# Performance work log

Hardware: AMD Instinct MI355X
Metric: run time of the kernel (lower is better)

Reference implementation:

```python
import jax, jax.numpy as jnp
import numpy as np

B, H, W, C = 32, 64, 64, 256


def setup_inputs() -> dict:
    key = jax.random.key(0)
    kq, kk, kv = jax.random.split(key, 3)
    query = jax.random.normal(kq, (B, H, W, C), dtype=jnp.float32)
    keys = jax.random.normal(kk, (B, H, W, C), dtype=jnp.float32)
    values = jax.random.normal(kv, (B, H, W, C), dtype=jnp.float32)
    return {"query": query, "keys": keys, "values": values}


def reference(query, keys, values):
    # A[b,q,k] = sum_{h,w} query[b,h,w,q] * keys[b,h,w,k]
    scores = jnp.einsum("bhwq,bhwk->bqk", query, keys)
    attn = jax.nn.softmax(scores, axis=-1)  # softmax over keys axis
    # out[b,q,h,w] = sum_k attn[b,q,k] * values[b,h,w,k]
    out = jnp.einsum("bqk,bhwk->bqhw", attn, values)
    return out
```

## Files before the change

kernel.cpp:

```cpp
#include <hip/hip_runtime.h>
#include <hip/hip_bf16.h>

#define B_  32
#define HW_ 4096
#define C_  256
#define S_LDS 40

using bf16x8 = __attribute__((ext_vector_type(8))) short;
using f32x4  = __attribute__((ext_vector_type(4))) float;
using u32x4  = __attribute__((ext_vector_type(4))) uint;

__device__ __forceinline__ ushort f2bf_rn(float x) {
    uint u = __builtin_bit_cast(uint, x);
    u += 0x7FFFu + ((u >> 16) & 1u);
    return (ushort)(u >> 16);
}
__device__ __forceinline__ uint pk_bf2(float a, float b) {
    return ((uint)f2bf_rn(b) << 16) | (uint)f2bf_rn(a);
}
__device__ __forceinline__ uint pk_rtz(float x0, float x1) {
    return __builtin_amdgcn_perm(__builtin_bit_cast(uint, x1),
                                 __builtin_bit_cast(uint, x0), 0x07060302u);
}
__device__ __forceinline__ void split2_rtz(float x0, float x1, uint& hi2, uint& lo2) {
    uint u0 = __builtin_bit_cast(uint, x0), u1 = __builtin_bit_cast(uint, x1);
    hi2 = __builtin_amdgcn_perm(u1, u0, 0x07060302u);
    float h0 = __builtin_bit_cast(float, u0 & 0xFFFF0000u);
    float h1 = __builtin_bit_cast(float, u1 & 0xFFFF0000u);
    lo2 = pk_rtz(x0 - h0, x1 - h1);
}

__global__ __launch_bounds__(256, 4) void scores_kernel(const float* __restrict__ qg,
                                                        const float* __restrict__ kg,
                                                        float* __restrict__ scores) {
    int x  = blockIdx.x;
    int s  = x & 7;
    int tn = (x >> 3) & 3;
    int tm = (x >> 5) & 1;
    int b  = x >> 6;

    __shared__ __align__(16) ushort Qhi[128 * S_LDS], Qlo[128 * S_LDS];
    __shared__ __align__(16) ushort Khi[64 * S_LDS],  Klo[64 * S_LDS];

    int tid = threadIdx.x, lane = tid & 63, w = tid >> 6;
    int m0 = (w >> 1) * 64;
    int n0 = (w & 1) * 32;
    int g = lane >> 4, r16 = lane & 15;

    int cq = tid & 127;
    int hq = (tid >> 7) * 16;
    int ck = tid & 63;
    int hk = (tid >> 6) * 8;

    const float* qcol = qg + (size_t)b * HW_ * C_ + tm * 128 + cq;
    const float* kcol = kg + (size_t)b * HW_ * C_ + tn * 64 + ck;

    f32x4 acc[4][2];
#pragma unroll
    for (int i = 0; i < 4; ++i)
#pragma unroll
        for (int j = 0; j < 2; ++j) acc[i][j] = (f32x4){0.f, 0.f, 0.f, 0.f};

#define LOAD_QK(qr, kr, itv) {                                                 \
        int hw0 = s * 512 + (itv) * 32;                                        \
        const float* qp = qcol + (size_t)(hw0 + hq) * C_;                      \
        _Pragma("unroll")                                                      \
        for (int j = 0; j < 16; ++j) qr[j] = qp[(size_t)j * C_];               \
        const float* kp = kcol + (size_t)(hw0 + hk) * C_;                      \
        _Pragma("unroll")                                                      \
        for (int j = 0; j < 8; ++j) kr[j] = kp[(size_t)j * C_];                \
    }

#define CONVERT_STORE(qr, kr) {                                                \
        uint qh[8], ql[8];                                                     \
        _Pragma("unroll")                                                      \
        for (int p = 0; p < 8; ++p) split2_rtz(qr[2*p], qr[2*p+1], qh[p], ql[p]); \
        int qb_ = cq * S_LDS + hq;                                             \
        *reinterpret_cast<u32x4*>(&Qhi[qb_])     = (u32x4){qh[0], qh[1], qh[2], qh[3]}; \
        *reinterpret_cast<u32x4*>(&Qhi[qb_ + 8]) = (u32x4){qh[4], qh[5], qh[6], qh[7]}; \
        *reinterpret_cast<u32x4*>(&Qlo[qb_])     = (u32x4){ql[0], ql[1], ql[2], ql[3]}; \
        *reinterpret_cast<u32x4*>(&Qlo[qb_ + 8]) = (u32x4){ql[4], ql[5], ql[6], ql[7]}; \
        uint kh[4], kl[4];                                                     \
        _Pragma("unroll")                                                      \
        for (int p = 0; p < 4; ++p) split2_rtz(kr[2*p], kr[2*p+1], kh[p], kl[p]); \
        int kb_ = ck * S_LDS + hk;                                             \
        *reinterpret_cast<u32x4*>(&Khi[kb_]) = (u32x4){kh[0], kh[1], kh[2], kh[3]}; \
        *reinterpret_cast<u32x4*>(&Klo[kb_]) = (u32x4){kl[0], kl[1], kl[2], kl[3]}; \
    }

#define MFMA_PHASE() {                                                         \
        __builtin_amdgcn_s_setprio(1);                                         \
        bf16x8 ahi[4], alo[4];                                                 \
        _Pragma("unroll")                                                      \
        for (int mi = 0; mi < 4; ++mi) {                                       \
            int off = (m0 + mi * 16 + r16) * S_LDS + g * 8;                    \
            ahi[mi] = *reinterpret_cast<const bf16x8*>(&Qhi[off]);             \
            alo[mi] = *reinterpret_cast<const bf16x8*>(&Qlo[off]);             \
        }                                                                      \
        _Pragma("unroll")                                                      \
        for (int ni = 0; ni < 2; ++ni) {                                       \
            int off = (n0 + ni * 16 + r16) * S_LDS + g * 8;                    \
            bf16x8 bhi = *reinterpret_cast<const bf16x8*>(&Khi[off]);          \
            bf16x8 blo = *reinterpret_cast<const bf16x8*>(&Klo[off]);          \
            _Pragma("unroll")                                                  \
            for (int mi = 0; mi < 4; ++mi) {                                   \
                acc[mi][ni] = __builtin_amdgcn_mfma_f32_16x16x32_bf16(ahi[mi], bhi, acc[mi][ni], 0, 0, 0); \
                acc[mi][ni] = __builtin_amdgcn_mfma_f32_16x16x32_bf16(ahi[mi], blo, acc[mi][ni], 0, 0, 0); \
                acc[mi][ni] = __builtin_amdgcn_mfma_f32_16x16x32_bf16(alo[mi], bhi, acc[mi][ni], 0, 0, 0); \
            }                                                                  \
        }                                                                      \
        __builtin_amdgcn_s_setprio(0);                                         \
    }

#define STEP(qc, kc, qn, kn, itv, doload) {                                    \
        if (doload) LOAD_QK(qn, kn, (itv) + 1);                                \
        __syncthreads();                                                       \
        CONVERT_STORE(qc, kc);                                                 \
        __syncthreads();                                                       \
        MFMA_PHASE();                                                          \
    }

    float qa[16], ka[8], qb[16], kb[8];
    LOAD_QK(qa, ka, 0);
    for (int p = 0; p < 8; ++p) {
        STEP(qa, ka, qb, kb, 2 * p, true);
        STEP(qb, kb, qa, ka, 2 * p + 1, p < 7);
    }

#pragma unroll
    for (int mi = 0; mi < 4; ++mi)
#pragma unroll
        for (int ni = 0; ni < 2; ++ni)
#pragma unroll
            for (int r = 0; r < 4; ++r) {
                int qrow = tm * 128 + m0 + mi * 16 + g * 4 + r;
                int kc   = tn * 64 + n0 + ni * 16 + r16;
                atomicAdd(&scores[((size_t)b * 256 + qrow) * 256 + kc], acc[mi][ni][r]);
            }
#undef STEP
#undef MFMA_PHASE
#undef CONVERT_STORE
#undef LOAD_QK
}

__global__ __launch_bounds__(256) void softmax_kernel(const float* __restrict__ scores,
                                                      ushort* __restrict__ attn) {
    int wid  = blockIdx.x * 4 + (threadIdx.x >> 6);
    int lane = threadIdx.x & 63;
    const float4 v = *reinterpret_cast<const float4*>(scores + (size_t)wid * 256 + lane * 4);
    float m = fmaxf(fmaxf(v.x, v.y), fmaxf(v.z, v.w));
#pragma unroll
    for (int off = 32; off; off >>= 1) m = fmaxf(m, __shfl_xor(m, off, 64));
    float e0 = __expf(v.x - m), e1 = __expf(v.y - m), e2 = __expf(v.z - m), e3 = __expf(v.w - m);
    float ssum = e0 + e1 + e2 + e3;
#pragma unroll
    for (int off = 32; off; off >>= 1) ssum += __shfl_xor(ssum, off, 64);
    float inv = 1.0f / ssum;
    uint2 o;
    o.x = pk_bf2(e0 * inv, e1 * inv);
    o.y = pk_bf2(e2 * inv, e3 * inv);
    *reinterpret_cast<uint2*>(attn + (size_t)wid * 256 + lane * 4) = o;
}

__global__ __launch_bounds__(256, 4) void pv_kernel(const ushort* __restrict__ attn,
                                                    const float* __restrict__ vg,
                                                    float* __restrict__ out) {
    int b   = blockIdx.x >> 6;
    int hw0 = (blockIdx.x & 63) * 64;
    int tid = threadIdx.x, lane = tid & 63, w = tid >> 6;
    int m0  = w * 64;
    int g   = lane >> 4, r16 = lane & 15;

    __shared__ __align__(16) float Vt[2 * 64 * 32];

    int srow = tid >> 2;
    int sslot = (tid & 3) * 2;
    int wi0 = srow * 32 + ((sslot ^ (srow & 7)) * 4);
    int wi1 = srow * 32 + (((sslot + 1) ^ (srow & 7)) * 4);
    const float* vstage = vg + ((size_t)(b * HW_ + hw0 + srow)) * C_ + sslot * 4;

    const ushort* abase = attn + (size_t)b * 256 * 256 + g * 8;

    f32x4 acc[4][4];
#pragma unroll
    for (int i = 0; i < 4; ++i)
#pragma unroll
        for (int j = 0; j < 4; ++j) acc[i][j] = (f32x4){0.f, 0.f, 0.f, 0.f};

    {
        f32x4 p0 = *reinterpret_cast<const f32x4*>(vstage);
        f32x4 p1 = *reinterpret_cast<const f32x4*>(vstage + 4);
        *reinterpret_cast<f32x4*>(&Vt[wi0]) = p0;
        *reinterpret_cast<f32x4*>(&Vt[wi1]) = p1;
    }
    __syncthreads();

    for (int p = 0; p < 8; ++p) {
        float* rbuf = &Vt[(p & 1) * 64 * 32];
        float* wbuf = &Vt[((p + 1) & 1) * 64 * 32];

        f32x4 n0v, n1v;
        if (p < 7) {
            n0v = *reinterpret_cast<const f32x4*>(vstage + (p + 1) * 32);
            n1v = *reinterpret_cast<const f32x4*>(vstage + (p + 1) * 32 + 4);
        }

        int k0 = p * 32;
        bf16x8 a[4];
#pragma unroll
        for (int mi = 0; mi < 4; ++mi)
            a[mi] = *reinterpret_cast<const bf16x8*>(abase + (size_t)(m0 + mi * 16 + r16) * 256 + k0);

#pragma unroll
        for (int ni = 0; ni < 4; ++ni) {
            int row = ni * 16 + r16, key = row & 7;
            f32x4 f0 = *reinterpret_cast<const f32x4*>(&rbuf[row * 32 + (((2 * g)     ^ key) * 4)]);
            f32x4 f1 = *reinterpret_cast<const f32x4*>(&rbuf[row * 32 + (((2 * g + 1) ^ key) * 4)]);
            bf16x8 bf = __builtin_bit_cast(bf16x8, (u32x4){
                pk_rtz(f0[0], f0[1]), pk_rtz(f0[2], f0[3]),
                pk_rtz(f1[0], f1[1]), pk_rtz(f1[2], f1[3])});
#pragma unroll
            for (int mi = 0; mi < 4; ++mi)
                acc[mi][ni] = __builtin_amdgcn_mfma_f32_16x16x32_bf16(a[mi], bf, acc[mi][ni], 0, 0, 0);
        }

        if (p < 7) {
            *reinterpret_cast<f32x4*>(&wbuf[wi0]) = n0v;
            *reinterpret_cast<f32x4*>(&wbuf[wi1]) = n1v;
            __syncthreads();
        }
    }

#pragma unroll
    for (int mi = 0; mi < 4; ++mi)
#pragma unroll
        for (int ni = 0; ni < 4; ++ni)
#pragma unroll
            for (int r = 0; r < 4; ++r) {
                int qrow = m0 + mi * 16 + g * 4 + r;
                int hw   = hw0 + ni * 16 + r16;
                out[((size_t)b * 256 + qrow) * 4096 + hw] = acc[mi][ni][r];
            }
}

extern "C" void kernel_launch(void* const* d_in, const int* in_sizes, int n_in,
                              void* d_out, int out_size, void* d_ws, size_t ws_size,
                              hipStream_t stream) {
    const float* q = (const float*)d_in[0];
    const float* k = (const float*)d_in[1];
    const float* v = (const float*)d_in[2];
    float* out = (float*)d_out;

    float*  scores = (float*)d_ws;
    ushort* attn   = (ushort*)((char*)d_ws + (size_t)B_ * 256 * 256 * 4);

    (void)hipMemsetAsync(d_ws, 0, (size_t)B_ * 256 * 256 * 4, stream);
    scores_kernel<<<2048, 256, 0, stream>>>(q, k, scores);
    softmax_kernel<<<2048, 256, 0, stream>>>(scores, attn);
    pv_kernel<<<2048, 256, 0, stream>>>(attn, v, out);
}
```

Before: 181.8 us.

## Replace atomic split-K reduction with per-slab stores summed in softmax

```diff
diff --git a/kernel.cpp b/kernel.cpp
--- a/kernel.cpp
+++ b/kernel.cpp
@@ -32,12 +32,13 @@
 
 __global__ __launch_bounds__(256, 4) void scores_kernel(const float* __restrict__ qg,
                                                         const float* __restrict__ kg,
-                                                        float* __restrict__ scores) {
+                                                        float* __restrict__ dst,
+                                                        long slabStride) {
     int x  = blockIdx.x;
-    int s  = x & 7;
-    int tn = (x >> 3) & 3;
-    int tm = (x >> 5) & 1;
-    int b  = x >> 6;
+    int s  = x & 3;
+    int tn = (x >> 2) & 3;
+    int tm = (x >> 4) & 1;
+    int b  = x >> 5;
 
     __shared__ __align__(16) ushort Qhi[128 * S_LDS], Qlo[128 * S_LDS];
     __shared__ __align__(16) ushort Khi[64 * S_LDS],  Klo[64 * S_LDS];
@@ -62,7 +63,7 @@
         for (int j = 0; j < 2; ++j) acc[i][j] = (f32x4){0.f, 0.f, 0.f, 0.f};
 
 #define LOAD_QK(qr, kr, itv) {                                                 \
-        int hw0 = s * 512 + (itv) * 32;                                        \
+        int hw0 = s * 1024 + (itv) * 32;                                       \
         const float* qp = qcol + (size_t)(hw0 + hq) * C_;                      \
         _Pragma("unroll")                                                      \
         for (int j = 0; j < 16; ++j) qr[j] = qp[(size_t)j * C_];               \
@@ -122,11 +123,12 @@
 
     float qa[16], ka[8], qb[16], kb[8];
     LOAD_QK(qa, ka, 0);
-    for (int p = 0; p < 8; ++p) {
+    for (int p = 0; p < 16; ++p) {
         STEP(qa, ka, qb, kb, 2 * p, true);
-        STEP(qb, kb, qa, ka, 2 * p + 1, p < 7);
-    }
-
+        STEP(qb, kb, qa, ka, 2 * p + 1, p < 15);
+    }
+
+    float* base = dst + (size_t)s * slabStride;
 #pragma unroll
     for (int mi = 0; mi < 4; ++mi)
 #pragma unroll
@@ -135,7 +137,9 @@
             for (int r = 0; r < 4; ++r) {
                 int qrow = tm * 128 + m0 + mi * 16 + g * 4 + r;
                 int kc   = tn * 64 + n0 + ni * 16 + r16;
-                atomicAdd(&scores[((size_t)b * 256 + qrow) * 256 + kc], acc[mi][ni][r]);
+                float* p = base + ((size_t)b * 256 + qrow) * 256 + kc;
+                if (slabStride) *p = acc[mi][ni][r];
+                else            atomicAdd(p, acc[mi][ni][r]);
             }
 #undef STEP
 #undef MFMA_PHASE
@@ -144,10 +148,16 @@
 }
 
 __global__ __launch_bounds__(256) void softmax_kernel(const float* __restrict__ scores,
-                                                      ushort* __restrict__ attn) {
+                                                      ushort* __restrict__ attn,
+                                                      int nslab, long slabStride) {
     int wid  = blockIdx.x * 4 + (threadIdx.x >> 6);
     int lane = threadIdx.x & 63;
-    const float4 v = *reinterpret_cast<const float4*>(scores + (size_t)wid * 256 + lane * 4);
+    const float* p0 = scores + (size_t)wid * 256 + lane * 4;
+    float4 v = *reinterpret_cast<const float4*>(p0);
+    for (int sl = 1; sl < nslab; ++sl) {
+        const float4 t = *reinterpret_cast<const float4*>(p0 + (size_t)sl * slabStride);
+        v.x += t.x; v.y += t.y; v.z += t.z; v.w += t.w;
+    }
     float m = fmaxf(fmaxf(v.x, v.y), fmaxf(v.z, v.w));
 #pragma unroll
     for (int off = 32; off; off >>= 1) m = fmaxf(m, __shfl_xor(m, off, 64));
@@ -251,11 +261,20 @@
     const float* v = (const float*)d_in[2];
     float* out = (float*)d_out;
 
-    float*  scores = (float*)d_ws;
-    ushort* attn   = (ushort*)((char*)d_ws + (size_t)B_ * 256 * 256 * 4);
-
-    (void)hipMemsetAsync(d_ws, 0, (size_t)B_ * 256 * 256 * 4, stream);
-    scores_kernel<<<2048, 256, 0, stream>>>(q, k, scores);
-    softmax_kernel<<<2048, 256, 0, stream>>>(scores, attn);
-    pv_kernel<<<2048, 256, 0, stream>>>(attn, v, out);
-}
+    const size_t slab = (size_t)B_ * 256 * 256;
+    const size_t needBytes = 4 * slab * 4 + slab * 2;
+    float* scores = (float*)d_ws;
+
+    if (ws_size >= needBytes) {
+        ushort* attn = (ushort*)((char*)d_ws + 4 * slab * 4);
+        scores_kernel<<<1024, 256, 0, stream>>>(q, k, scores, (long)slab);
+        softmax_kernel<<<2048, 256, 0, stream>>>(scores, attn, 4, (long)slab);
+        pv_kernel<<<2048, 256, 0, stream>>>(attn, v, out);
+    } else {
+        ushort* attn = (ushort*)((char*)d_ws + slab * 4);
+        (void)hipMemsetAsync(d_ws, 0, slab * 4, stream);
+        scores_kernel<<<1024, 256, 0, stream>>>(q, k, scores, 0L);
+        softmax_kernel<<<2048, 256, 0, stream>>>(scores, attn, 1, 0L);
+        pv_kernel<<<2048, 256, 0, stream>>>(attn, v, out);
+    }
+}
```

Result: faster. 176.2 us, median of 2 (-3.1%).
